# Optimization experiments

Hardware: AMD Instinct MI355X
Metric: run time of the kernel (lower is better)

## Reference

```python
import math
import jax, jax.numpy as jnp
import numpy as np

N_ORDERS = 2
CHUNK = 64  # tokens per chunk (before virtual-token expansion)


def _expand_derivative(x, n):
    """expand_virtual_tokens(mode='derivative'): [B,H,S,D] -> [B,H,S*n,D]."""
    B, H, S, D = x.shape
    pad = jnp.zeros((B, H, n - 1, D), x.dtype)
    xp = jnp.concatenate([pad, x], axis=2)  # [B,H,S+n-1,D]
    coeffs = np.array([(-1) ** kk * math.comb(n - 1, kk) for kk in range(n)], dtype=np.float32)
    coeffs = coeffs / np.abs(coeffs).sum()  # L1-normalized binomial coeffs
    # window j at token t is x_pad[t+j]*coeffs[j]; then flip window dim (as in torch .flip(-1))
    win = jnp.stack([xp[:, :, j:j + S, :] * coeffs[j] for j in range(n)], axis=3)  # [B,H,S,n,D]
    win = win[:, :, :, ::-1, :]
    return win.reshape(B, H, S * n, D)


def _unlinear(x, scale=2.0):
    """unlinear_activation: gated norm-scaled gelu applied to inter-chunk state."""
    xn = jnp.linalg.norm(x, axis=-1, keepdims=True) + 1e-6
    return x / scale * jax.nn.gelu(scale * x / xn, approximate=True)


def _stab(x):
    # ensure_stability: clamp to [-1e4, 1e4], nan -> center (0)
    return jnp.nan_to_num(jnp.clip(x, -1e4, 1e4), nan=0.0, posinf=1e4, neginf=-1e4)


def _forward(q, k, v, beta):
    n = N_ORDERS
    B, H, S, D = q.shape
    qe = _expand_derivative(q, n)
    ke = _expand_derivative(k, n)
    ve = _expand_derivative(v, n)
    be = jnp.repeat(beta, n, axis=-1)[..., None]  # [B,H,S*n,1]
    w = ke * be  # delta-rule write keys
    u = ve * be  # delta-rule write values

    Cn = CHUNK * n                     # virtual tokens per chunk
    NC = (S * n) // Cn                 # number of chunks
    ch = lambda x: x.reshape(B, H, NC, Cn, D)
    qc, kc, wc, uc = ch(qe), ch(ke), ch(w), ch(u)

    # triangular (forward-substitution) inversion per chunk:
    # T = (I + tril(W K^T, -1))^{-1}  == fast_invert_matrix of the strictly-lower system
    A = jnp.tril(jnp.einsum('bhnid,bhnjd->bhnij', wc, kc), -1)
    eye = jnp.eye(Cn, dtype=q.dtype)
    T = jax.scipy.linalg.solve_triangular(
        eye + A, jnp.broadcast_to(eye, A.shape), lower=True, unit_diagonal=True)
    wci = jnp.einsum('bhnij,bhnjd->bhnid', T, wc)
    uci = jnp.einsum('bhnij,bhnjd->bhnid', T, uc)

    def chunk_step(h, xs):
        # sequential_delta_product_scan body: per-token Householder updates, n_orders steps
        qx, wx, ux = xs  # each [B,H,Cn,D]
        C = CHUNK
        qr = qx.reshape(B, H, C, n, D)
        wr = wx.reshape(B, H, C, n, D)
        ur = ux.reshape(B, H, C, n, D)
        state = jnp.broadcast_to(h[:, :, None], (B, H, C, D, D))  # per-token state
        outs = []
        for s in range(n):
            qs, ws, us = qr[:, :, :, s], wr[:, :, :, s], ur[:, :, :, s]
            kho = jnp.einsum('bhcd,bhcde->bhce', ws, state)
            uval = us - kho
            o_inter = jnp.einsum('bhcd,bhcde->bhce', qs, state)
            o_intra = qs * uval
            state = _stab(state + jnp.einsum('bhcd,bhce->bhcde', ws, uval))
            outs.append(o_intra + o_inter)
        o = jnp.stack(outs, axis=3).reshape(B, H, C * n, D)  # interleave: pos t*n+s
        h_new = _unlinear(state[:, :, -1])  # linear_activation=False path
        return h_new, o

    xs = (jnp.moveaxis(qc, 2, 0), jnp.moveaxis(wci, 2, 0), jnp.moveaxis(uci, 2, 0))
    h0 = jnp.zeros((B, H, D, D), q.dtype)
    _, os = jax.lax.scan(chunk_step, h0, xs)  # os: [NC,B,H,Cn,D]
    out_v = jnp.moveaxis(os, 0, 2).reshape(B, H, S, n, D)
    return out_v[..., n - 1, :]  # collapse virtual tokens: keep last-order output per token


def setup_inputs() -> dict:
    key = jax.random.key(0)
    kq, kk, kv, kb = jax.random.split(key, 4)
    B, H, S, D = 2, 16, 2048, 64
    return {
        'q': jax.random.normal(kq, (B, H, S, D), jnp.float32),
        'k': jax.random.normal(kk, (B, H, S, D), jnp.float32),
        'v': jax.random.normal(kv, (B, H, S, D), jnp.float32),
        'beta': jax.random.uniform(kb, (B, H, S), jnp.float32),
    }


def reference(q, k, v, beta):
    return _forward(q, k, v, beta)
```

## Files before the change

kernel.cpp:

```cpp
#include <hip/hip_runtime.h>
#include <math.h>


namespace {
constexpr int PAIRS = 32;
constexpr int SLEN  = 2048;
constexpr int D     = 64;
constexpr int CK    = 64;
constexpr int CN    = 128;
constexpr int NCH   = 32;
constexpr int NB2   = 8;

__device__ __forceinline__ float stab1(float x) {
    float y = __builtin_amdgcn_fmed3f(x, -10000.f, 10000.f);
    return (x != x) ? 0.f : y;
}

__device__ __forceinline__ int kidx(int a, int f4) {
    return a * 68 + 4 * (f4 ^ ((a >> 2) & 3));
}
}

__global__ __launch_bounds__(256, 2)
void la_phase1(const float* __restrict__ kg, const float* __restrict__ vg,
               const float* __restrict__ bg, float* __restrict__ ws)
{
    __shared__ float Ysh[CN][64];
    __shared__ float Gm[65][66];
    __shared__ char  ureg[17680];
    __shared__ float bq4[CK], bh[CK];

    float* kstf = (float*)ureg;
    float* scm  = (float*)ureg;
    float (*redsh)[66] = (float(*)[66])(ureg + 8192);

    const int blk  = blockIdx.x;
    const int p    = blk >> 6;
    const int nc   = (blk >> 1) & 31;
    const int half = blk & 1;
    const int tid  = threadIdx.x;
    const int lane = tid & 63;
    const int m    = tid >> 6;
    const int baseT = nc * CK;
    const float* kp = kg + (size_t)p * SLEN * D;
    const float* vp = vg + (size_t)p * SLEN * D;
    const float* bp = bg + (size_t)p * SLEN;

    for (int u = tid; u < 65 * 16; u += 256) {
        int a = u >> 4, f4 = u & 15;
        int src = baseT - 1 + a;
        float4 val = float4{0.f, 0.f, 0.f, 0.f};
        if (src >= 0) val = ((const float4*)(kp + (size_t)src * D))[f4];
        *(float4*)&kstf[kidx(a, f4)] = val;
    }
    if (tid < CK) {
        float bv = bp[baseT + tid];
        bq4[tid] = 0.25f * bv;
        bh[tid]  = 0.5f  * bv;
    }
    __syncthreads();

    for (int u = tid; u < CN * 16; u += 256) {
        int i = u >> 4, f4 = u & 15;
        int ci = i >> 1, si = i & 1;
        float sc = si ? bh[ci] : -bh[ci];
        float4 val = float4{0.f, 0.f, 0.f, 0.f};
        if (half == 0) {
            int ai = ci - si + 1;
            val = *(const float4*)&kstf[kidx(ai, f4)];
        } else {
            int srcT = baseT + ci - si;
            if (srcT >= 0) val = ((const float4*)(vp + (size_t)srcT * D))[f4];
        }
        val.x *= sc; val.y *= sc; val.z *= sc; val.w *= sc;
        *(float4*)&Ysh[i][f4 * 4] = val;
    }

    for (int tt = tid; tt < 17 * 17; tt += 256) {
        int ta = tt / 17, tb = tt % 17;
        if (tb > ta) continue;
        int a0 = ta * 4, b0 = tb * 4;
        float acc[4][4] = {};
        for (int d4 = 0; d4 < 16; ++d4) {
            float4 av[4], bv[4];
            #pragma unroll
            for (int r = 0; r < 4; ++r) {
                av[r] = *(const float4*)&kstf[kidx(min(a0 + r, 64), d4)];
                bv[r] = *(const float4*)&kstf[kidx(min(b0 + r, 64), d4)];
            }
            #pragma unroll
            for (int r = 0; r < 4; ++r)
                #pragma unroll
                for (int c = 0; c < 4; ++c)
                    acc[r][c] += av[r].x * bv[c].x + av[r].y * bv[c].y
                               + av[r].z * bv[c].z + av[r].w * bv[c].w;
        }
        #pragma unroll
        for (int r = 0; r < 4; ++r)
            #pragma unroll
            for (int c = 0; c < 4; ++c)
                if (a0 + r <= 64 && b0 + c <= 64) {
                    Gm[a0 + r][b0 + c] = acc[r][c];
                    Gm[b0 + c][a0 + r] = acc[r][c];
                }
    }
    __syncthreads();

    auto stripf = [&](int g, int t0, int tstride) {
        int buf = g & 1;
        int jmax = 8 * g + 8;
        for (int e = t0; e < 8 * jmax; e += tstride) {
            int j = e >> 3, r = e & 7;
            int i = 8 * g + r;
            int ai = (i >> 1) - (i & 1) + 1;
            int aj = (j >> 1) - (j & 1) + 1;
            float sgn = ((i ^ j) & 1) ? -1.f : 1.f;
            scm[(buf * CN + j) * 8 + r] = sgn * bq4[i >> 1] * Gm[ai][aj];
        }
    };

    stripf(0, tid, 256);
    __syncthreads();

    const int col = lane;
    for (int g = 0; g < 16; ++g) {
        const int buf = g & 1;
        float acc[8] = {};
        for (int j = m; j < 8 * g; j += 4) {
            float yv = Ysh[j][col];
            const float4 a03 = *(const float4*)&scm[(buf * CN + j) * 8];
            const float4 a47 = *(const float4*)&scm[(buf * CN + j) * 8 + 4];
            acc[0] += a03.x * yv; acc[1] += a03.y * yv;
            acc[2] += a03.z * yv; acc[3] += a03.w * yv;
            acc[4] += a47.x * yv; acc[5] += a47.y * yv;
            acc[6] += a47.z * yv; acc[7] += a47.w * yv;
        }
        if (m > 0) {
            #pragma unroll
            for (int r = 0; r < 8; ++r) redsh[(m - 1) * 8 + r][col] = acc[r];
        }
        __syncthreads();
        if (m == 0) {
            float yn[8];
            #pragma unroll
            for (int r = 0; r < 8; ++r) {
                float val = Ysh[8 * g + r][col] - acc[r]
                          - redsh[r][col] - redsh[8 + r][col] - redsh[16 + r][col];
                #pragma unroll
                for (int rp = 0; rp < 8; ++rp)
                    if (rp < r) val -= scm[(buf * CN + 8 * g + rp) * 8 + r] * yn[rp];
                yn[r] = val;
                Ysh[8 * g + r][col] = val;
            }
        } else if (g < 15) {
            stripf(g + 1, tid - 64, 192);
        }
        __syncthreads();
    }

    float* gY = ws + (size_t)(p * NCH + nc) * (CN * CN) + half * 64;
    for (int u = tid; u < CN * 16; u += 256) {
        int r = u >> 4, f4 = u & 15;
        *(float4*)&gY[r * CN + f4 * 4] = *(const float4*)&Ysh[r][f4 * 4];
    }
}

__global__ __launch_bounds__(512)
void la_phase2(const float* __restrict__ qg, const float* __restrict__ ws,
               float* __restrict__ outg)
{
    __shared__ float WU[2][9][256];
    __shared__ float Qs[2][9][64];
    __shared__ float partA[8][9][64];
    __shared__ float partB[8][9][64];
    __shared__ float UV0[9][64];
    __shared__ float UV1r[64];

    const int blk  = blockIdx.x;
    const int p    = blk >> 3, nb = blk & 7;
    const int tid  = threadIdx.x;
    const int w    = tid >> 6, lane = tid & 63;

    const float* qp = qg + (size_t)p * SLEN * D;
    float* op = outg + (size_t)p * SLEN * D;
    const float* wsbase = ws + (size_t)p * NCH * (CN * CN);

    const int cMain = nb * 8 + w;

    float4 wuR = float4{0.f, 0.f, 0.f, 0.f};
    float  qR  = 0.f;
    float4 wuR2 = float4{0.f, 0.f, 0.f, 0.f};
    float  qR2  = 0.f;

    auto stage_load = [&](int nc) {
        const float* gY = wsbase + (size_t)nc * (CN * CN);
        wuR = *(const float4*)(gY + (size_t)(2 * cMain) * CN + lane * 4);
        int t = nc * CK + cMain;
        int srcT = (t > 0) ? t - 1 : 0;
        qR = qp[(size_t)srcT * D + lane];
        if (w == 0) {
            wuR2 = *(const float4*)(gY + (size_t)(2 * 63) * CN + lane * 4);
            qR2 = qp[(size_t)(nc * CK + 62) * D + lane];
        }
    };
    auto stage_write = [&](int buf) {
        *(float4*)&WU[buf][w][lane * 4] = wuR;
        Qs[buf][w][lane] = qR;
        if (w == 0) {
            *(float4*)&WU[buf][8][lane * 4] = wuR2;
            Qs[buf][8][lane] = qR2;
        }
    };

    float hs[8];
    #pragma unroll
    for (int j = 0; j < 8; ++j) hs[j] = 0.f;

    stage_load(0);
    stage_write(0);
    __syncthreads();

    for (int nc = 0; nc < NCH; ++nc) {
        const int buf = nc & 1;
        if (nc + 1 < NCH) stage_load(nc + 1);

        #pragma unroll
        for (int P = 0; P < 9; ++P) {
            float4 a = *(const float4*)&WU[buf][P][8 * w];
            float4 b = *(const float4*)&WU[buf][P][8 * w + 4];
            float s = ((a.x * hs[0] + a.y * hs[1]) + (a.z * hs[2] + a.w * hs[3]))
                    + ((b.x * hs[4] + b.y * hs[5]) + (b.z * hs[6] + b.w * hs[7]));
            partA[w][P][lane] = s;
        }
        __syncthreads();

        {
            float s = 0.f;
            #pragma unroll
            for (int wv = 0; wv < 8; ++wv) s += partA[wv][w][lane];
            UV0[w][lane] = WU[buf][w][64 + lane] - s;
        }
        if (w == 0) {
            float s = 0.f;
            #pragma unroll
            for (int wv = 0; wv < 8; ++wv) s += partA[wv][8][lane];
            UV0[8][lane] = WU[buf][8][64 + lane] - s;
        }
        __syncthreads();

        #pragma unroll
        for (int P = 0; P < 9; ++P) {
            float uv0 = UV0[P][lane];
            float4 w0a = *(const float4*)&WU[buf][P][8 * w];
            float4 w0b = *(const float4*)&WU[buf][P][8 * w + 4];
            float4 w1a = *(const float4*)&WU[buf][P][128 + 8 * w];
            float4 w1b = *(const float4*)&WU[buf][P][128 + 8 * w + 4];
            float4 qa  = *(const float4*)&Qs[buf][P][8 * w];
            float4 qb  = *(const float4*)&Qs[buf][P][8 * w + 4];
            float st0 = stab1(hs[0] + w0a.x * uv0);
            float st1 = stab1(hs[1] + w0a.y * uv0);
            float st2 = stab1(hs[2] + w0a.z * uv0);
            float st3 = stab1(hs[3] + w0a.w * uv0);
            float st4 = stab1(hs[4] + w0b.x * uv0);
            float st5 = stab1(hs[5] + w0b.y * uv0);
            float st6 = stab1(hs[6] + w0b.z * uv0);
            float st7 = stab1(hs[7] + w0b.w * uv0);
            float kh = ((w1a.x * st0 + w1a.y * st1) + (w1a.z * st2 + w1a.w * st3))
                     + ((w1b.x * st4 + w1b.y * st5) + (w1b.z * st6 + w1b.w * st7));
            float oa = ((qa.x * st0 + qa.y * st1) + (qa.z * st2 + qa.w * st3))
                     + ((qb.x * st4 + qb.y * st5) + (qb.z * st6 + qb.w * st7));
            partA[w][P][lane] = kh;
            partB[w][P][lane] = oa;
        }
        __syncthreads();

        {
            float skh = 0.f, soa = 0.f;
            #pragma unroll
            for (int wv = 0; wv < 8; ++wv) {
                skh += partA[wv][w][lane];
                soa += partB[wv][w][lane];
            }
            float uv1 = WU[buf][w][192 + lane] - skh;
            int t = nc * CK + cMain;
            float qlane = Qs[buf][w][lane];
            float outv = 0.5f * (qlane * uv1 + soa);
            op[(size_t)t * D + lane] = (t > 0) ? outv : 0.f;
        }
        if (w == 0) {
            float skh = 0.f;
            #pragma unroll
            for (int wv = 0; wv < 8; ++wv) skh += partA[wv][8][lane];
            UV1r[lane] = WU[buf][8][192 + lane] - skh;
        }
        __syncthreads();

        {
            float uv0l = UV0[8][lane];
            float uv1l = UV1r[lane];
            float4 w0a = *(const float4*)&WU[buf][8][8 * w];
            float4 w0b = *(const float4*)&WU[buf][8][8 * w + 4];
            float4 w1a = *(const float4*)&WU[buf][8][128 + 8 * w];
            float4 w1b = *(const float4*)&WU[buf][8][128 + 8 * w + 4];
            float st2v[8], ss[8];
            st2v[0] = stab1(stab1(hs[0] + w0a.x * uv0l) + w1a.x * uv1l);
            st2v[1] = stab1(stab1(hs[1] + w0a.y * uv0l) + w1a.y * uv1l);
            st2v[2] = stab1(stab1(hs[2] + w0a.z * uv0l) + w1a.z * uv1l);
            st2v[3] = stab1(stab1(hs[3] + w0a.w * uv0l) + w1a.w * uv1l);
            st2v[4] = stab1(stab1(hs[4] + w0b.x * uv0l) + w1b.x * uv1l);
            st2v[5] = stab1(stab1(hs[5] + w0b.y * uv0l) + w1b.y * uv1l);
            st2v[6] = stab1(stab1(hs[6] + w0b.z * uv0l) + w1b.z * uv1l);
            st2v[7] = stab1(stab1(hs[7] + w0b.w * uv0l) + w1b.w * uv1l);
            #pragma unroll
            for (int j = 0; j < 8; ++j) ss[j] = st2v[j] * st2v[j];
            #pragma unroll
            for (int msk = 1; msk < 64; msk <<= 1) {
                #pragma unroll
                for (int j = 0; j < 8; ++j) ss[j] += __shfl_xor(ss[j], msk);
            }
            #pragma unroll
            for (int j = 0; j < 8; ++j) {
                float xn = __builtin_amdgcn_sqrtf(ss[j]) + 1e-6f;
                float y  = 2.f * st2v[j] * __builtin_amdgcn_rcpf(xn);
                float y2 = y * y;
                float e  = __builtin_amdgcn_exp2f(y * (2.3022078f + 0.1029432f * y2));
                float th = (e - 1.f) * __builtin_amdgcn_rcpf(e + 1.f);
                hs[j] = 0.25f * st2v[j] * y * (1.f + th);
            }
        }

        if (nc + 1 < NCH) stage_write(buf ^ 1);
        __syncthreads();
    }
}

extern "C" void kernel_launch(void* const* d_in, const int* in_sizes, int n_in,
                              void* d_out, int out_size, void* d_ws, size_t ws_size,
                              hipStream_t stream)
{
    (void)in_sizes; (void)n_in; (void)out_size; (void)ws_size;
    const float* q    = (const float*)d_in[0];
    const float* k    = (const float*)d_in[1];
    const float* v    = (const float*)d_in[2];
    const float* beta = (const float*)d_in[3];
    float* ws  = (float*)d_ws;
    float* out = (float*)d_out;

    la_phase1<<<PAIRS * NCH * 2, 256, 0, stream>>>(k, v, beta, ws);
    la_phase2<<<PAIRS * NB2, 512, 0, stream>>>(q, ws, out);
}
```

Baseline: 300.1 us.

## Merge phase1 halves into one block, pipeline solve strips, split phase2 finer

Phase 1 now processes both the K and V halves of a chunk in a single 512-thread block, so the Gram matrix and coefficient strips are computed once instead of twice. The forward-substitution loop is restructured so one warp group finalizes rows while three others precompute partial sums and the coefficient strip two steps ahead, using triple buffering, which cuts barrier-bound serial work. Phase 2 doubles its block count, with each block covering 4 tokens instead of 8, to raise parallelism and occupancy for the sequential scan, at the cost of redundant state recomputation per block. The risks are lower occupancy in phase 1 and duplicated state work in phase 2.

```diff
diff --git a/kernel.cpp b/kernel.cpp
--- a/kernel.cpp
+++ b/kernel.cpp
@@ -9,7 +9,8 @@
 constexpr int CK    = 64;
 constexpr int CN    = 128;
 constexpr int NCH   = 32;
-constexpr int NB2   = 8;
+constexpr int NB2   = 16;
+constexpr int NP    = 5;
 
 __device__ __forceinline__ float stab1(float x) {
     float y = __builtin_amdgcn_fmed3f(x, -10000.f, 10000.f);
@@ -21,32 +22,29 @@
 }
 }
 
-__global__ __launch_bounds__(256, 2)
+__global__ __launch_bounds__(512, 1)
 void la_phase1(const float* __restrict__ kg, const float* __restrict__ vg,
                const float* __restrict__ bg, float* __restrict__ ws)
 {
-    __shared__ float Ysh[CN][64];
+    __shared__ float Ysh[CN][CN];
     __shared__ float Gm[65][66];
-    __shared__ char  ureg[17680];
+    __shared__ char  ureg[36864];
     __shared__ float bq4[CK], bh[CK];
 
     float* kstf = (float*)ureg;
     float* scm  = (float*)ureg;
-    float (*redsh)[66] = (float(*)[66])(ureg + 8192);
+    float (*redsh)[3][8][CN] = (float(*)[3][8][CN])(ureg + 12288);
 
     const int blk  = blockIdx.x;
-    const int p    = blk >> 6;
-    const int nc   = (blk >> 1) & 31;
-    const int half = blk & 1;
+    const int p    = blk >> 5;
+    const int nc   = blk & 31;
     const int tid  = threadIdx.x;
-    const int lane = tid & 63;
-    const int m    = tid >> 6;
     const int baseT = nc * CK;
     const float* kp = kg + (size_t)p * SLEN * D;
     const float* vp = vg + (size_t)p * SLEN * D;
     const float* bp = bg + (size_t)p * SLEN;
 
-    for (int u = tid; u < 65 * 16; u += 256) {
+    for (int u = tid; u < 65 * 16; u += 512) {
         int a = u >> 4, f4 = u & 15;
         int src = baseT - 1 + a;
         float4 val = float4{0.f, 0.f, 0.f, 0.f};
@@ -60,23 +58,22 @@
     }
     __syncthreads();
 
-    for (int u = tid; u < CN * 16; u += 256) {
-        int i = u >> 4, f4 = u & 15;
+    for (int u = tid; u < CN * 32; u += 512) {
+        int i = u >> 5, f4i = u & 31;
         int ci = i >> 1, si = i & 1;
         float sc = si ? bh[ci] : -bh[ci];
         float4 val = float4{0.f, 0.f, 0.f, 0.f};
-        if (half == 0) {
-            int ai = ci - si + 1;
-            val = *(const float4*)&kstf[kidx(ai, f4)];
+        if (f4i < 16) {
+            val = *(const float4*)&kstf[kidx(ci - si + 1, f4i)];
         } else {
             int srcT = baseT + ci - si;
-            if (srcT >= 0) val = ((const float4*)(vp + (size_t)srcT * D))[f4];
+            if (srcT >= 0) val = ((const float4*)(vp + (size_t)srcT * D))[f4i - 16];
         }
         val.x *= sc; val.y *= sc; val.z *= sc; val.w *= sc;
-        *(float4*)&Ysh[i][f4 * 4] = val;
-    }
-
-    for (int tt = tid; tt < 17 * 17; tt += 256) {
+        *(float4*)&Ysh[i][f4i * 4] = val;
+    }
+
+    for (int tt = tid; tt < 17 * 17; tt += 512) {
         int ta = tt / 17, tb = tt % 17;
         if (tb > ta) continue;
         int a0 = ta * 4, b0 = tb * 4;
@@ -106,78 +103,106 @@
     }
     __syncthreads();
 
-    auto stripf = [&](int g, int t0, int tstride) {
-        int buf = g & 1;
-        int jmax = 8 * g + 8;
-        for (int e = t0; e < 8 * jmax; e += tstride) {
-            int j = e >> 3, r = e & 7;
-            int i = 8 * g + r;
-            int ai = (i >> 1) - (i & 1) + 1;
-            int aj = (j >> 1) - (j & 1) + 1;
-            float sgn = ((i ^ j) & 1) ? -1.f : 1.f;
-            scm[(buf * CN + j) * 8 + r] = sgn * bq4[i >> 1] * Gm[ai][aj];
-        }
-    };
-
-    stripf(0, tid, 256);
+    for (int e = tid; e < 192; e += 512) {
+        int gp = (e < 64) ? 0 : 1;
+        int ee = e - gp * 64;
+        int j = ee >> 3, r = ee & 7;
+        int i = 8 * gp + r;
+        int ai = (i >> 1) - (i & 1) + 1;
+        int aj = (j >> 1) - (j & 1) + 1;
+        float sgn = ((i ^ j) & 1) ? -1.f : 1.f;
+        scm[(gp * CN + j) * 8 + r] = sgn * bq4[i >> 1] * Gm[ai][aj];
+    }
     __syncthreads();
 
-    const int col = lane;
+    const int col = tid & 127;
+    const int grp = tid >> 7;
+
     for (int g = 0; g < 16; ++g) {
-        const int buf = g & 1;
-        float acc[8] = {};
-        for (int j = m; j < 8 * g; j += 4) {
-            float yv = Ysh[j][col];
-            const float4 a03 = *(const float4*)&scm[(buf * CN + j) * 8];
-            const float4 a47 = *(const float4*)&scm[(buf * CN + j) * 8 + 4];
-            acc[0] += a03.x * yv; acc[1] += a03.y * yv;
-            acc[2] += a03.z * yv; acc[3] += a03.w * yv;
-            acc[4] += a47.x * yv; acc[5] += a47.y * yv;
-            acc[6] += a47.z * yv; acc[7] += a47.w * yv;
-        }
-        if (m > 0) {
-            #pragma unroll
-            for (int r = 0; r < 8; ++r) redsh[(m - 1) * 8 + r][col] = acc[r];
-        }
-        __syncthreads();
-        if (m == 0) {
+        const int bufG  = g % 3;
+        const int bufG1 = (g + 1) % 3;
+        const int bufG2 = (g + 2) % 3;
+
+        if (grp == 0) {
+            float acc[8] = {};
+            if (g > 0) {
+                #pragma unroll
+                for (int r = 0; r < 8; ++r)
+                    acc[r] = redsh[g & 1][0][r][col] + redsh[g & 1][1][r][col]
+                           + redsh[g & 1][2][r][col];
+                #pragma unroll
+                for (int jj = 0; jj < 8; ++jj) {
+                    int j = 8 * g - 8 + jj;
+                    float yv = Ysh[j][col];
+                    const float4 a03 = *(const float4*)&scm[(bufG * CN + j) * 8];
+                    const float4 a47 = *(const float4*)&scm[(bufG * CN + j) * 8 + 4];
+                    acc[0] += a03.x * yv; acc[1] += a03.y * yv;
+                    acc[2] += a03.z * yv; acc[3] += a03.w * yv;
+                    acc[4] += a47.x * yv; acc[5] += a47.y * yv;
+                    acc[6] += a47.z * yv; acc[7] += a47.w * yv;
+                }
+            }
             float yn[8];
             #pragma unroll
             for (int r = 0; r < 8; ++r) {
-                float val = Ysh[8 * g + r][col] - acc[r]
-                          - redsh[r][col] - redsh[8 + r][col] - redsh[16 + r][col];
+                float val = Ysh[8 * g + r][col] - acc[r];
                 #pragma unroll
                 for (int rp = 0; rp < 8; ++rp)
-                    if (rp < r) val -= scm[(buf * CN + 8 * g + rp) * 8 + r] * yn[rp];
+                    if (rp < r) val -= scm[(bufG * CN + 8 * g + rp) * 8 + r] * yn[rp];
                 yn[r] = val;
                 Ysh[8 * g + r][col] = val;
             }
-        } else if (g < 15) {
-            stripf(g + 1, tid - 64, 192);
-        }
-        __syncthreads();
-    }
-
-    float* gY = ws + (size_t)(p * NCH + nc) * (CN * CN) + half * 64;
-    for (int u = tid; u < CN * 16; u += 256) {
-        int r = u >> 4, f4 = u & 15;
+        } else {
+            if (g + 2 <= 15) {
+                int gb = g + 2, jmax = 8 * gb + 8;
+                for (int e = tid - 128; e < 8 * jmax; e += 384) {
+                    int j = e >> 3, r = e & 7;
+                    int i = 8 * gb + r;
+                    int ai = (i >> 1) - (i & 1) + 1;
+                    int aj = (j >> 1) - (j & 1) + 1;
+                    float sgn = ((i ^ j) & 1) ? -1.f : 1.f;
+                    scm[(bufG2 * CN + j) * 8 + r] = sgn * bq4[i >> 1] * Gm[ai][aj];
+                }
+            }
+            if (g + 1 <= 15) {
+                float acc[8] = {};
+                for (int j = grp - 1; j < 8 * g; j += 3) {
+                    float yv = Ysh[j][col];
+                    const float4 a03 = *(const float4*)&scm[(bufG1 * CN + j) * 8];
+                    const float4 a47 = *(const float4*)&scm[(bufG1 * CN + j) * 8 + 4];
+                    acc[0] += a03.x * yv; acc[1] += a03.y * yv;
+                    acc[2] += a03.z * yv; acc[3] += a03.w * yv;
+                    acc[4] += a47.x * yv; acc[5] += a47.y * yv;
+                    acc[6] += a47.z * yv; acc[7] += a47.w * yv;
+                }
+                #pragma unroll
+                for (int r = 0; r < 8; ++r)
+                    redsh[(g + 1) & 1][grp - 1][r][col] = acc[r];
+            }
+        }
+        __syncthreads();
+    }
+
+    float* gY = ws + (size_t)(p * NCH + nc) * (CN * CN);
+    for (int u = tid; u < CN * 32; u += 512) {
+        int r = u >> 5, f4 = u & 31;
         *(float4*)&gY[r * CN + f4 * 4] = *(const float4*)&Ysh[r][f4 * 4];
     }
 }
 
-__global__ __launch_bounds__(512)
+__global__ __launch_bounds__(512, 2)
 void la_phase2(const float* __restrict__ qg, const float* __restrict__ ws,
                float* __restrict__ outg)
 {
-    __shared__ float WU[2][9][256];
-    __shared__ float Qs[2][9][64];
-    __shared__ float partA[8][9][64];
-    __shared__ float partB[8][9][64];
-    __shared__ float UV0[9][64];
+    __shared__ float WU[2][NP][256];
+    __shared__ float Qs[2][NP][64];
+    __shared__ float partA[8][NP][64];
+    __shared__ float partB[8][NP][64];
+    __shared__ float UV0[NP][64];
     __shared__ float UV1r[64];
 
     const int blk  = blockIdx.x;
-    const int p    = blk >> 3, nb = blk & 7;
+    const int p    = blk >> 4, nb = blk & 15;
     const int tid  = threadIdx.x;
     const int w    = tid >> 6, lane = tid & 63;
 
@@ -185,30 +210,26 @@
     float* op = outg + (size_t)p * SLEN * D;
     const float* wsbase = ws + (size_t)p * NCH * (CN * CN);
 
-    const int cMain = nb * 8 + w;
+    const int cMain = nb * 4 + w;
 
     float4 wuR = float4{0.f, 0.f, 0.f, 0.f};
     float  qR  = 0.f;
-    float4 wuR2 = float4{0.f, 0.f, 0.f, 0.f};
-    float  qR2  = 0.f;
 
     auto stage_load = [&](int nc) {
         const float* gY = wsbase + (size_t)nc * (CN * CN);
-        wuR = *(const float4*)(gY + (size_t)(2 * cMain) * CN + lane * 4);
-        int t = nc * CK + cMain;
-        int srcT = (t > 0) ? t - 1 : 0;
-        qR = qp[(size_t)srcT * D + lane];
-        if (w == 0) {
-            wuR2 = *(const float4*)(gY + (size_t)(2 * 63) * CN + lane * 4);
-            qR2 = qp[(size_t)(nc * CK + 62) * D + lane];
+        if (w < 4) {
+            wuR = *(const float4*)(gY + (size_t)(2 * cMain) * CN + lane * 4);
+            int t = nc * CK + cMain;
+            qR = qp[(size_t)((t > 0) ? t - 1 : 0) * D + lane];
+        } else if (w == 4) {
+            wuR = *(const float4*)(gY + (size_t)126 * CN + lane * 4);
+            qR = qp[(size_t)(nc * CK + 62) * D + lane];
         }
     };
     auto stage_write = [&](int buf) {
-        *(float4*)&WU[buf][w][lane * 4] = wuR;
-        Qs[buf][w][lane] = qR;
-        if (w == 0) {
-            *(float4*)&WU[buf][8][lane * 4] = wuR2;
-            Qs[buf][8][lane] = qR2;
+        if (w < NP) {
+            *(float4*)&WU[buf][w][lane * 4] = wuR;
+            Qs[buf][w][lane] = qR;
         }
     };
 
@@ -225,7 +246,7 @@
         if (nc + 1 < NCH) stage_load(nc + 1);
 
         #pragma unroll
-        for (int P = 0; P < 9; ++P) {
+        for (int P = 0; P < NP; ++P) {
             float4 a = *(const float4*)&WU[buf][P][8 * w];
             float4 b = *(const float4*)&WU[buf][P][8 * w + 4];
             float s = ((a.x * hs[0] + a.y * hs[1]) + (a.z * hs[2] + a.w * hs[3]))
@@ -234,22 +255,16 @@
         }
         __syncthreads();
 
-        {
+        if (w < NP) {
             float s = 0.f;
             #pragma unroll
             for (int wv = 0; wv < 8; ++wv) s += partA[wv][w][lane];
             UV0[w][lane] = WU[buf][w][64 + lane] - s;
         }
-        if (w == 0) {
-            float s = 0.f;
-            #pragma unroll
-            for (int wv = 0; wv < 8; ++wv) s += partA[wv][8][lane];
-            UV0[8][lane] = WU[buf][8][64 + lane] - s;
-        }
         __syncthreads();
 
         #pragma unroll
-        for (int P = 0; P < 9; ++P) {
+        for (int P = 0; P < NP; ++P) {
             float uv0 = UV0[P][lane];
             float4 w0a = *(const float4*)&WU[buf][P][8 * w];
             float4 w0b = *(const float4*)&WU[buf][P][8 * w + 4];
@@ -274,7 +289,7 @@
         }
         __syncthreads();
 
-        {
+        if (w < 4) {
             float skh = 0.f, soa = 0.f;
             #pragma unroll
             for (int wv = 0; wv < 8; ++wv) {
@@ -283,25 +298,23 @@
             }
             float uv1 = WU[buf][w][192 + lane] - skh;
             int t = nc * CK + cMain;
-            float qlane = Qs[buf][w][lane];
-            float outv = 0.5f * (qlane * uv1 + soa);
+            float outv = 0.5f * (Qs[buf][w][lane] * uv1 + soa);
             op[(size_t)t * D + lane] = (t > 0) ? outv : 0.f;
-        }
-        if (w == 0) {
+        } else if (w == 4) {
             float skh = 0.f;
             #pragma unroll
-            for (int wv = 0; wv < 8; ++wv) skh += partA[wv][8][lane];
-            UV1r[lane] = WU[buf][8][192 + lane] - skh;
+            for (int wv = 0; wv < 8; ++wv) skh += partA[wv][4][lane];
+            UV1r[lane] = WU[buf][4][192 + lane] - skh;
         }
         __syncthreads();
 
         {
-            float uv0l = UV0[8][lane];
+            float uv0l = UV0[4][lane];
             float uv1l = UV1r[lane];
-            float4 w0a = *(const float4*)&WU[buf][8][8 * w];
-            float4 w0b = *(const float4*)&WU[buf][8][8 * w + 4];
-            float4 w1a = *(const float4*)&WU[buf][8][128 + 8 * w];
-            float4 w1b = *(const float4*)&WU[buf][8][128 + 8 * w + 4];
+            float4 w0a = *(const float4*)&WU[buf][4][8 * w];
+            float4 w0b = *(const float4*)&WU[buf][4][8 * w + 4];
+            float4 w1a = *(const float4*)&WU[buf][4][128 + 8 * w];
+            float4 w1b = *(const float4*)&WU[buf][4][128 + 8 * w + 4];
             float st2v[8], ss[8];
             st2v[0] = stab1(stab1(hs[0] + w0a.x * uv0l) + w1a.x * uv1l);
             st2v[1] = stab1(stab1(hs[1] + w0a.y * uv0l) + w1a.y * uv1l);
@@ -346,6 +359,6 @@
     float* ws  = (float*)d_ws;
     float* out = (float*)d_out;
 
-    la_phase1<<<PAIRS * NCH * 2, 256, 0, stream>>>(k, v, beta, ws);
+    la_phase1<<<PAIRS * NCH, 512, 0, stream>>>(k, v, beta, ws);
     la_phase2<<<PAIRS * NB2, 512, 0, stream>>>(q, ws, out);
 }
```

Result: slower. 320.6 us (+6.8%).
